# Kernel optimization log

Hardware: AMD Instinct MI355X
Metric: run time of the kernel (lower is better)

The kernel has to match this reference:

```python
import jax, jax.numpy as jnp
import numpy as np

N = 50000
E = 800000
NODE_F = 5
MAP_F = 32
EDGE_F = 4
HID = 64
RNN = 20
RNN_E = 8
LAT = 32
OUT = 4


def setup_inputs() -> dict:
    key = jax.random.key(0)
    ks = iter(jax.random.split(key, 40))
    def rn(shape, scale=0.1):
        return jax.random.normal(next(ks), shape, dtype=jnp.float32) * scale
    inp = {
        "x": rn((N, NODE_F), 1.0),
        "u": rn((N, MAP_F), 1.0),
        "edge_index": jax.random.randint(next(ks), (2, E), 0, N, dtype=jnp.int32),
        "edge_attr": rn((E, EDGE_F), 1.0),
        "h_node_h": rn((N, RNN), 1.0),
        "h_node_c": rn((N, RNN), 1.0),
        "h_edge_h": rn((N, RNN_E), 1.0),
        "h_edge_c": rn((N, RNN_E), 1.0),
        # node-history LSTM (input = node_features + map_encoding_size = 37)
        "W_ih_n": rn((4 * RNN, NODE_F + MAP_F)), "W_hh_n": rn((4 * RNN, RNN)),
        "b_ih_n": jnp.zeros((4 * RNN,), jnp.float32), "b_hh_n": jnp.zeros((4 * RNN,), jnp.float32),
        # edge-history LSTM (input = latent_edge_features)
        "W_ih_e": rn((4 * RNN_E, LAT)), "W_hh_e": rn((4 * RNN_E, RNN_E)),
        "b_ih_e": jnp.zeros((4 * RNN_E,), jnp.float32), "b_hh_e": jnp.zeros((4 * RNN_E,), jnp.float32),
        # message edge MLP: in = 2*37 + 4 = 78 -> 64 -> 32
        "We1": rn((2 * (NODE_F + MAP_F) + EDGE_F, HID)), "be1": jnp.zeros((HID,), jnp.float32),
        "We2": rn((HID, LAT)), "be2": jnp.zeros((LAT,), jnp.float32),
        # GN_out edge MLP: in = 2*(rnn_size + rnn_edge_size) + 4 = 60 -> 64 -> 32
        "Wo1": rn((2 * (RNN + RNN_E) + EDGE_F, HID)), "bo1": jnp.zeros((HID,), jnp.float32),
        "Wo2": rn((HID, LAT)), "bo2": jnp.zeros((LAT,), jnp.float32),
        # GN_out node MLP: in = (rnn_size + rnn_edge_size) + latent = 60 -> 64 -> 4
        "Wn1": rn((RNN + RNN_E + LAT, HID)), "bn1": jnp.zeros((HID,), jnp.float32),
        "Wn2": rn((HID, OUT)), "bn2": jnp.zeros((OUT,), jnp.float32),
    }
    return inp


def _lstm_step(xin, h, c, Wih, Whh, bih, bhh):
    # torch gate order: i, f, g, o
    g = xin @ Wih.T + h @ Whh.T + bih + bhh
    i, f, gg, o = jnp.split(g, 4, axis=-1)
    c_new = jax.nn.sigmoid(f) * c + jax.nn.sigmoid(i) * jnp.tanh(gg)
    h_new = jax.nn.sigmoid(o) * jnp.tanh(c_new)
    return h_new, c_new


def _segment_mean(vals, idx, n):
    s = jax.ops.segment_sum(vals, idx, num_segments=n)
    cnt = jax.ops.segment_sum(jnp.ones((vals.shape[0], 1), vals.dtype), idx, num_segments=n)
    return s / jnp.maximum(cnt, 1.0)


def _edge_mlp(src, dst, edge_attr, W1, b1, W2, b2):
    h = jnp.concatenate([src, dst, edge_attr], axis=-1)
    return jax.nn.relu(h @ W1 + b1) @ W2 + b2


def reference(x, u, edge_index, edge_attr, h_node_h, h_node_c, h_edge_h, h_edge_c,
              W_ih_n, W_hh_n, b_ih_n, b_hh_n, W_ih_e, W_hh_e, b_ih_e, b_hh_e,
              We1, be1, We2, be2, Wo1, bo1, Wo2, bo2, Wn1, bn1, Wn2, bn2):
    n = x.shape[0]
    xu = jnp.concatenate([x, u], axis=-1)  # [N, 37]
    # node history RNN step
    node_hist, node_c = _lstm_step(xu, h_node_h, h_node_c, W_ih_n, W_hh_n, b_ih_n, b_hh_n)
    # message GN: gather -> edge MLP
    row, col = edge_index[0], edge_index[1]
    messages = _edge_mlp(xu[row], xu[col], edge_attr, We1, be1, We2, be2)  # [E, 32]
    # edge history RNN: aggregate messages per receiving node, then LSTM step
    agg_msg = _segment_mean(messages, col, n)  # [N, 32]
    edge_hist, edge_c = _lstm_step(agg_msg, h_edge_h, h_edge_c, W_ih_e, W_hh_e, b_ih_e, b_hh_e)
    # output GN block
    full = jnp.concatenate([node_hist, edge_hist], axis=-1)  # [N, 28]
    e2 = _edge_mlp(full[row], full[col], edge_attr, Wo1, bo1, Wo2, bo2)  # [E, 32]
    agg2 = _segment_mean(e2, col, n)  # [N, 32]
    node_in = jnp.concatenate([full, agg2], axis=-1)  # [N, 60]
    out = jax.nn.relu(node_in @ Wn1 + bn1) @ Wn2 + bn2  # [N, 4]
    return (out, node_hist, node_c, edge_hist, edge_c)
```

## Files before the change

kernel.cpp:

```cpp
#include <hip/hip_runtime.h>
#include <math.h>

#define NN 50000
#define EE 800000
#define SBLK ((NN + 255) / 256)

typedef short bf16x8 __attribute__((ext_vector_type(8)));
typedef float f32x4 __attribute__((ext_vector_type(4)));
typedef unsigned short ushort_t;
#define MFMA16(a, b, c) __builtin_amdgcn_mfma_f32_16x16x32_bf16(a, b, c, 0, 0, 0)

__device__ __forceinline__ float sigmoidf_(float x) { return 1.0f / (1.0f + __expf(-x)); }

__device__ __forceinline__ unsigned short f2bf(float f) {
    unsigned u = __builtin_bit_cast(unsigned, f);
    u += 0x7FFFu + ((u >> 16) & 1u);
    return (unsigned short)(u >> 16);
}
__device__ __forceinline__ float bf2f(unsigned short v) {
    unsigned u = (unsigned)v << 16;
    return __builtin_bit_cast(float, u);
}
__device__ __forceinline__ unsigned pk2(float a, float b) {
    return ((unsigned)f2bf(b) << 16) | (unsigned)f2bf(a);
}

#define W1ST_A 104
#define W1ST_B 72
#define C1ST_  72
#define PW1A (64 * W1ST_A)
#define PW2A (32 * C1ST_)
#define PW1B (64 * W1ST_B)
#define PW2B (32 * C1ST_)

__global__ __launch_bounds__(256) void pack_w_k(
    const float* __restrict__ We1, const float* __restrict__ We2,
    const float* __restrict__ Wo1, const float* __restrict__ Wo2,
    ushort_t* __restrict__ pw)
{
    ushort_t* pw1a = pw;
    ushort_t* pw2a = pw1a + PW1A;
    ushort_t* pw1b = pw2a + PW2A;
    ushort_t* pw2b = pw1b + PW1B;
    int tid = threadIdx.x;

    for (int i = tid; i < PW1A; i += 256) {
        int n = i / W1ST_A, nk = i - n * W1ST_A;
        int kp = 0; bool z = false;
        if (nk < 37) kp = nk;
        else if (nk < 40) z = true;
        else if (nk < 77) kp = nk - 3;
        else if (nk < 80) z = true;
        else if (nk < 84) kp = nk - 6;
        else z = true;
        pw1a[i] = z ? (ushort_t)0 : f2bf(We1[kp * 64 + n]);
    }
    for (int i = tid; i < PW2A; i += 256) {
        int n = i / C1ST_, k = i - n * C1ST_;
        pw2a[i] = (k < 64) ? f2bf(We2[k * 32 + n]) : (ushort_t)0;
    }
    for (int i = tid; i < PW1B; i += 256) {
        int n = i / W1ST_B, nk = i - n * W1ST_B;
        int kp = 0; bool z = false;
        if (nk < 28) kp = nk;
        else if (nk < 32) z = true;
        else if (nk < 64) kp = nk - 4;
        else z = true;
        pw1b[i] = z ? (ushort_t)0 : f2bf(Wo1[kp * 64 + n]);
    }
    for (int i = tid; i < PW2B; i += 256) {
        int n = i / C1ST_, k = i - n * C1ST_;
        pw2b[i] = (k < 64) ? f2bf(Wo2[k * 32 + n]) : (ushort_t)0;
    }
}

__global__ __launch_bounds__(256) void node_lstm_k(
    const float* __restrict__ x, const float* __restrict__ u,
    const float* __restrict__ h0, const float* __restrict__ c0,
    const float* __restrict__ Wih, const float* __restrict__ Whh,
    const float* __restrict__ bih, const float* __restrict__ bhh,
    ushort_t* __restrict__ xu16, float* __restrict__ h_out, float* __restrict__ c_out)
{
    __shared__ float sWih[80 * 37];
    __shared__ float sWhh[80 * 20];
    __shared__ float sb[80];
    for (int i = threadIdx.x; i < 80 * 37; i += 256) sWih[i] = Wih[i];
    for (int i = threadIdx.x; i < 80 * 20; i += 256) sWhh[i] = Whh[i];
    if (threadIdx.x < 80) sb[threadIdx.x] = bih[threadIdx.x] + bhh[threadIdx.x];
    __syncthreads();
    int n = blockIdx.x * 256 + threadIdx.x;
    if (n >= NN) return;

    float xu[40];
#pragma unroll
    for (int k = 0; k < 5; k++) xu[k] = x[n * 5 + k];
#pragma unroll
    for (int k = 0; k < 32; k++) xu[5 + k] = u[n * 32 + k];
    xu[37] = 0.f; xu[38] = 0.f; xu[39] = 0.f;

    {
        unsigned w[20];
#pragma unroll
        for (int k = 0; k < 20; k++) w[k] = pk2(xu[2 * k], xu[2 * k + 1]);
        uint4* dst = (uint4*)(xu16 + (size_t)n * 40);
#pragma unroll
        for (int q = 0; q < 5; q++)
            dst[q] = make_uint4(w[q * 4], w[q * 4 + 1], w[q * 4 + 2], w[q * 4 + 3]);
    }

    float h[20];
#pragma unroll
    for (int k = 0; k < 20; k++) h[k] = h0[n * 20 + k];

#pragma unroll 1
    for (int r = 0; r < 20; r++) {
        float gi = sb[r], gf = sb[20 + r], gg = sb[40 + r], go = sb[60 + r];
#pragma unroll
        for (int k = 0; k < 37; k++) {
            float v = xu[k];
            gi = fmaf(v, sWih[r * 37 + k], gi);
            gf = fmaf(v, sWih[(20 + r) * 37 + k], gf);
            gg = fmaf(v, sWih[(40 + r) * 37 + k], gg);
            go = fmaf(v, sWih[(60 + r) * 37 + k], go);
        }
#pragma unroll
        for (int k = 0; k < 20; k++) {
            float v = h[k];
            gi = fmaf(v, sWhh[r * 20 + k], gi);
            gf = fmaf(v, sWhh[(20 + r) * 20 + k], gf);
            gg = fmaf(v, sWhh[(40 + r) * 20 + k], gg);
            go = fmaf(v, sWhh[(60 + r) * 20 + k], go);
        }
        float cr = c0[n * 20 + r];
        float cn = sigmoidf_(gf) * cr + sigmoidf_(gi) * tanhf(gg);
        float hn = sigmoidf_(go) * tanhf(cn);
        h_out[n * 20 + r] = hn;
        c_out[n * 20 + r] = cn;
    }
}

__global__ __launch_bounds__(256) void csr_count_k(const int* __restrict__ col,
                                                   int* __restrict__ count)
{
    int e = blockIdx.x * 256 + threadIdx.x;
    if (e < EE) atomicAdd(&count[col[e]], 1);
}

__global__ __launch_bounds__(256) void scan1_k(const int* __restrict__ count,
                                               int* __restrict__ bsum)
{
    __shared__ int red[256];
    int t = threadIdx.x;
    int i = blockIdx.x * 256 + t;
    red[t] = (i < NN) ? count[i] : 0;
    __syncthreads();
#pragma unroll
    for (int d = 128; d > 0; d >>= 1) {
        if (t < d) red[t] += red[t + d];
        __syncthreads();
    }
    if (t == 0) bsum[blockIdx.x] = red[0];
}

__global__ __launch_bounds__(256) void scan2_k(const int* __restrict__ bsum,
                                               int* __restrict__ bpre)
{
    __shared__ int s[256];
    int t = threadIdx.x;
    int v = (t < SBLK) ? bsum[t] : 0;
    s[t] = v;
    __syncthreads();
#pragma unroll
    for (int d = 1; d < 256; d <<= 1) {
        int w = (t >= d) ? s[t - d] : 0;
        __syncthreads();
        s[t] += w;
        __syncthreads();
    }
    if (t < SBLK) bpre[t] = s[t] - v;
}

__global__ __launch_bounds__(256) void scan3_k(const int* __restrict__ count,
                                               const int* __restrict__ bpre,
                                               int* __restrict__ offset,
                                               float* __restrict__ cntf)
{
    __shared__ int s[256];
    int t = threadIdx.x;
    int i = blockIdx.x * 256 + t;
    int v = (i < NN) ? count[i] : 0;
    s[t] = v;
    __syncthreads();
#pragma unroll
    for (int d = 1; d < 256; d <<= 1) {
        int w = (t >= d) ? s[t - d] : 0;
        __syncthreads();
        s[t] += w;
        __syncthreads();
    }
    if (i < NN) {
        offset[i] = bpre[blockIdx.x] + s[t] - v;
        cntf[i] = (float)v;
    }
}

__global__ __launch_bounds__(256) void csr_fill4_k(const int* __restrict__ row,
                                                   const int* __restrict__ col,
                                                   const float* __restrict__ eattr,
                                                   const int* __restrict__ offset,
                                                   int* __restrict__ cursor,
                                                   uint4* __restrict__ edat)
{
    int e = blockIdx.x * 256 + threadIdx.x;
    if (e >= EE) return;
    int c = col[e];
    int pos = atomicAdd(&cursor[c], 1);
    int slot = offset[c] + pos;
    float4 ev = *(const float4*)&eattr[(size_t)e * 4];
    edat[slot] = make_uint4((unsigned)row[e], (unsigned)c, pk2(ev.x, ev.y), pk2(ev.z, ev.w));
}

template <int F, int STRIDE, int INK>
__global__ __launch_bounds__(256, 4) void edge_mlp_fused_k(
    const ushort_t* __restrict__ feat,
    const uint4* __restrict__ edat,
    const int* __restrict__ offset, const int* __restrict__ count,
    const ushort_t* __restrict__ pw,
    const float* __restrict__ b1, const float* __restrict__ b2,
    float* __restrict__ agg)
{
    constexpr int S1 = INK / 32;
    constexpr int W1ST = INK + 8;
    constexpr int C1ST = C1ST_;
    constexpr int ABYTES = (64 * W1ST + 32 * C1ST + 4 * 32 * C1ST) * 2;
    constexpr int BBYTES = 32 * 257 * 4;
    constexpr int UBYTES = (ABYTES > BBYTES) ? ABYTES : BBYTES;
    constexpr int NU4 = (64 * W1ST + 32 * C1ST) / 8;

    __shared__ __align__(16) char ldsu[UBYTES];
    __shared__ int colLds[256];
    __shared__ unsigned char segStartA[256];
    __shared__ short segEndA[256];
    __shared__ int segCnt;

    ushort_t* sW1 = (ushort_t*)ldsu;
    ushort_t* sW2 = sW1 + 64 * W1ST;
    ushort_t* sC1 = sW2 + 32 * C1ST;
    float*    msgT = (float*)ldsu;

    const int tid = threadIdx.x;
    const int B0 = blockIdx.x * 256;
    if (tid == 0) segCnt = 0;
    colLds[tid] = (int)edat[B0 + tid].y;

    {
        const uint4* src = (const uint4*)pw;
        uint4* dst = (uint4*)ldsu;
        for (int i = tid; i < NU4; i += 256) dst[i] = src[i];
    }
    __syncthreads();

    {
        bool isStart = (tid == 0) || (colLds[tid] != colLds[tid - 1]);
        if (isStart) {
            int node = colLds[tid];
            int off = offset[node], cn = count[node];
            int e = off + cn - B0; if (e > 256) e = 256;
            bool fullseg = (off >= B0) && (off + cn <= B0 + 256);
            int j = atomicAdd(&segCnt, 1);
            segStartA[j] = (unsigned char)tid;
            segEndA[j] = (short)(fullseg ? -e : e);
        }
    }

    const int wave = tid >> 6, lane = tid & 63;
    const int lr = lane & 15, jb = lane >> 4;
    const size_t slotBase = (size_t)B0 + (size_t)wave * 64;
    const float4* b1v = (const float4*)b1;
    ushort_t* myC1 = sC1 + wave * 32 * C1ST;
    const float bb2_0 = b2[lr], bb2_1 = b2[16 + lr];

    f32x4 acc2a[2][2][2];

#pragma unroll
    for (int half = 0; half < 2; half++) {
        bf16x8 xf[2][S1];
#pragma unroll
        for (int ne2 = 0; ne2 < 2; ne2++) {
            size_t slot = slotBase + (size_t)(half * 2 + ne2) * 16 + lr;
            uint4 ed = edat[slot];
            const ushort_t* xr = feat + (size_t)ed.x * STRIDE;
            const ushort_t* xc = feat + (size_t)ed.y * STRIDE;
            xf[ne2][0] = *(const bf16x8*)(xr + jb * 8);
            if (F == 37) {
                const ushort_t* p1 = (jb == 0) ? (xr + 32) : (xc + (jb - 1) * 8);
                xf[ne2][1] = *(const bf16x8*)p1;
                bf16x8 v;
                if (jb < 2) {
                    v = *(const bf16x8*)((jb == 0) ? (xc + 24) : (xc + 32));
                } else if (jb == 2) {
                    uint4 t = make_uint4(ed.z, ed.w, 0u, 0u);
                    v = __builtin_bit_cast(bf16x8, t);
                } else {
                    uint4 t = make_uint4(0u, 0u, 0u, 0u);
                    v = __builtin_bit_cast(bf16x8, t);
                }
                xf[ne2][2] = v;
            } else {
                if (jb < 3) {
                    xf[ne2][1] = *(const bf16x8*)(xc + jb * 8);
                } else {
                    uint2 lo = *(const uint2*)(xc + 24);
                    uint4 t = make_uint4(lo.x, lo.y, ed.z, ed.w);
                    xf[ne2][1] = __builtin_bit_cast(bf16x8, t);
                }
            }
        }

        f32x4 acc1[4][2];
#pragma unroll
        for (int mh = 0; mh < 4; mh++) {
            float4 bv = b1v[mh * 4 + jb];
            f32x4 bi = {bv.x, bv.y, bv.z, bv.w};
            acc1[mh][0] = bi; acc1[mh][1] = bi;
        }
#pragma unroll
        for (int s = 0; s < S1; s++) {
#pragma unroll
            for (int mh = 0; mh < 4; mh++) {
                bf16x8 wf = *(const bf16x8*)&sW1[(mh * 16 + lr) * W1ST + s * 32 + jb * 8];
                acc1[mh][0] = MFMA16(wf, xf[0][s], acc1[mh][0]);
                acc1[mh][1] = MFMA16(wf, xf[1][s], acc1[mh][1]);
            }
        }

#pragma unroll
        for (int mh = 0; mh < 4; mh++) {
#pragma unroll
            for (int ne2 = 0; ne2 < 2; ne2++) {
                f32x4 a = acc1[mh][ne2];
                unsigned w0 = pk2(fmaxf(a[0], 0.f), fmaxf(a[1], 0.f));
                unsigned w1 = pk2(fmaxf(a[2], 0.f), fmaxf(a[3], 0.f));
                *(uint2*)&myC1[(ne2 * 16 + lr) * C1ST + mh * 16 + jb * 4] = make_uint2(w0, w1);
            }
        }

#pragma unroll
        for (int m = 0; m < 2; m++) {
            acc2a[half][m][0] = f32x4{bb2_0, bb2_0, bb2_0, bb2_0};
            acc2a[half][m][1] = f32x4{bb2_1, bb2_1, bb2_1, bb2_1};
        }
#pragma unroll
        for (int s2 = 0; s2 < 2; s2++) {
            bf16x8 w2f0 = *(const bf16x8*)&sW2[lr * C1ST + s2 * 32 + jb * 8];
            bf16x8 w2f1 = *(const bf16x8*)&sW2[(16 + lr) * C1ST + s2 * 32 + jb * 8];
#pragma unroll
            for (int m = 0; m < 2; m++) {
                bf16x8 a2 = *(const bf16x8*)&myC1[(m * 16 + lr) * C1ST + s2 * 32 + jb * 8];
                acc2a[half][m][0] = MFMA16(a2, w2f0, acc2a[half][m][0]);
                acc2a[half][m][1] = MFMA16(a2, w2f1, acc2a[half][m][1]);
            }
        }
    }

    __syncthreads();
#pragma unroll
    for (int half = 0; half < 2; half++) {
#pragma unroll
        for (int m = 0; m < 2; m++) {
            int row = wave * 64 + (half * 2 + m) * 16 + jb * 4;
#pragma unroll
            for (int n = 0; n < 2; n++) {
                f32x4 a = acc2a[half][m][n];
                float* dst = &msgT[(size_t)(n * 16 + lr) * 257 + row];
                dst[0] = a[0]; dst[1] = a[1]; dst[2] = a[2]; dst[3] = a[3];
            }
        }
    }
    __syncthreads();

    {
        int f = lane & 31;
        int h = lane >> 5;
        const float* mrow = msgT + (size_t)f * 257;
        int nseg = segCnt;
        for (int j = wave; j < nseg; j += 4) {
            int s = segStartA[j];
            int ev = segEndA[j];
            bool fullseg = ev < 0;
            int e = fullseg ? -ev : ev;
            int node = colLds[s];
            float sum = 0.f;
            for (int i = s + h; i < e; i += 2) sum += mrow[i];
            sum += __shfl_xor(sum, 32);
            if (lane < 32) {
                float* dst = &agg[(size_t)node * 32 + f];
                if (fullseg) *dst = sum;
                else atomicAdd(dst, sum);
            }
        }
    }
}

__global__ __launch_bounds__(256) void edge_lstm_k(
    const float* __restrict__ agg, const float* __restrict__ cnt,
    const float* __restrict__ h0, const float* __restrict__ c0,
    const float* __restrict__ Wih, const float* __restrict__ Whh,
    const float* __restrict__ bih, const float* __restrict__ bhh,
    const float* __restrict__ node_h,
    float* __restrict__ h_out, float* __restrict__ c_out, ushort_t* __restrict__ full16)
{
    __shared__ float sWih[32 * 32];
    __shared__ float sWhh[32 * 8];
    __shared__ float sb[32];
    for (int i = threadIdx.x; i < 32 * 32; i += 256) sWih[i] = Wih[i];
    for (int i = threadIdx.x; i < 32 * 8; i += 256) sWhh[i] = Whh[i];
    if (threadIdx.x < 32) sb[threadIdx.x] = bih[threadIdx.x] + bhh[threadIdx.x];
    __syncthreads();
    int n = blockIdx.x * 256 + threadIdx.x;
    if (n >= NN) return;

    float inv = 1.0f / fmaxf(cnt[n], 1.0f);
    float msg[32];
#pragma unroll
    for (int k = 0; k < 32; k++) msg[k] = agg[(size_t)n * 32 + k] * inv;
    float h[8];
#pragma unroll
    for (int k = 0; k < 8; k++) h[k] = h0[n * 8 + k];

    float fl[32];
#pragma unroll
    for (int k = 0; k < 20; k++) fl[k] = node_h[n * 20 + k];
    fl[28] = 0.f; fl[29] = 0.f; fl[30] = 0.f; fl[31] = 0.f;

#pragma unroll
    for (int r = 0; r < 8; r++) {
        float gi = sb[r], gf = sb[8 + r], gg = sb[16 + r], go = sb[24 + r];
#pragma unroll
        for (int k = 0; k < 32; k++) {
            float v = msg[k];
            gi = fmaf(v, sWih[r * 32 + k], gi);
            gf = fmaf(v, sWih[(8 + r) * 32 + k], gf);
            gg = fmaf(v, sWih[(16 + r) * 32 + k], gg);
            go = fmaf(v, sWih[(24 + r) * 32 + k], go);
        }
#pragma unroll
        for (int k = 0; k < 8; k++) {
            float v = h[k];
            gi = fmaf(v, sWhh[r * 8 + k], gi);
            gf = fmaf(v, sWhh[(8 + r) * 8 + k], gf);
            gg = fmaf(v, sWhh[(16 + r) * 8 + k], gg);
            go = fmaf(v, sWhh[(24 + r) * 8 + k], go);
        }
        float cr = c0[n * 8 + r];
        float cn = sigmoidf_(gf) * cr + sigmoidf_(gi) * tanhf(gg);
        float hn = sigmoidf_(go) * tanhf(cn);
        h_out[n * 8 + r] = hn;
        c_out[n * 8 + r] = cn;
        fl[20 + r] = hn;
    }
    unsigned w[16];
#pragma unroll
    for (int k = 0; k < 16; k++) w[k] = pk2(fl[2 * k], fl[2 * k + 1]);
    uint4* dst = (uint4*)(full16 + (size_t)n * 32);
#pragma unroll
    for (int q = 0; q < 4; q++)
        dst[q] = make_uint4(w[q * 4], w[q * 4 + 1], w[q * 4 + 2], w[q * 4 + 3]);
}

__global__ __launch_bounds__(256) void node_out_k(
    const ushort_t* __restrict__ full16, const float* __restrict__ agg2, const float* __restrict__ cnt,
    const float* __restrict__ W1, const float* __restrict__ b1,
    const float* __restrict__ W2, const float* __restrict__ b2,
    float* __restrict__ out)
{
    __shared__ __align__(16) float sW1[60 * 64];
    __shared__ __align__(16) float sW2[64 * 4];
    __shared__ float sb1[64];
    __shared__ float sb2[4];
    for (int i = threadIdx.x; i < 60 * 64; i += 256) sW1[i] = W1[i];
    for (int i = threadIdx.x; i < 64 * 4; i += 256) sW2[i] = W2[i];
    if (threadIdx.x < 64) sb1[threadIdx.x] = b1[threadIdx.x];
    if (threadIdx.x < 4) sb2[threadIdx.x] = b2[threadIdx.x];
    __syncthreads();
    int n = blockIdx.x * 256 + threadIdx.x;
    if (n >= NN) return;

    float in[60];
    const ushort_t* fr = full16 + (size_t)n * 32;
#pragma unroll
    for (int k = 0; k < 28; k++) in[k] = bf2f(fr[k]);
    float inv = 1.0f / fmaxf(cnt[n], 1.0f);
#pragma unroll
    for (int k = 0; k < 32; k++) in[28 + k] = agg2[(size_t)n * 32 + k] * inv;

    float o[4] = {sb2[0], sb2[1], sb2[2], sb2[3]};
#pragma unroll 1
    for (int j = 0; j < 64; j += 4) {
        float s[4] = {sb1[j], sb1[j + 1], sb1[j + 2], sb1[j + 3]};
#pragma unroll
        for (int k = 0; k < 60; k++) {
            float4 w = *(const float4*)&sW1[k * 64 + j];
            s[0] = fmaf(in[k], w.x, s[0]);
            s[1] = fmaf(in[k], w.y, s[1]);
            s[2] = fmaf(in[k], w.z, s[2]);
            s[3] = fmaf(in[k], w.w, s[3]);
        }
#pragma unroll
        for (int jj = 0; jj < 4; jj++) {
            float sv = fmaxf(s[jj], 0.0f);
            float4 w = *(const float4*)&sW2[(j + jj) * 4];
            o[0] = fmaf(sv, w.x, o[0]);
            o[1] = fmaf(sv, w.y, o[1]);
            o[2] = fmaf(sv, w.z, o[2]);
            o[3] = fmaf(sv, w.w, o[3]);
        }
    }
#pragma unroll
    for (int m = 0; m < 4; m++) out[n * 4 + m] = o[m];
}

template <int F, int STRIDE, bool DO_CNT>
__global__ __launch_bounds__(256) void edge_mlp_atomic_k(
    const ushort_t* __restrict__ feat,
    const int* __restrict__ row, const int* __restrict__ col,
    const float* __restrict__ eattr,
    const float* __restrict__ W1, const float* __restrict__ b1,
    const float* __restrict__ W2, const float* __restrict__ b2,
    float* __restrict__ agg, float* __restrict__ cnt)
{
    constexpr int IN = 2 * F + 4;
    __shared__ __align__(16) float sW1[IN * 64];
    __shared__ __align__(16) float sW2[64 * 32];
    __shared__ float sb1[64];
    __shared__ float sb2[32];
    for (int i = threadIdx.x; i < IN * 64; i += 256) sW1[i] = W1[i];
    for (int i = threadIdx.x; i < 64 * 32; i += 256) sW2[i] = W2[i];
    if (threadIdx.x < 64) sb1[threadIdx.x] = b1[threadIdx.x];
    if (threadIdx.x < 32) sb2[threadIdx.x] = b2[threadIdx.x];
    __syncthreads();
    int e = blockIdx.x * 256 + threadIdx.x;
    if (e >= EE) return;

    int r = row[e], c = col[e];
    float h[IN];
#pragma unroll
    for (int k = 0; k < F; k++) h[k] = bf2f(feat[(size_t)r * STRIDE + k]);
#pragma unroll
    for (int k = 0; k < F; k++) h[F + k] = bf2f(feat[(size_t)c * STRIDE + k]);
    float4 ev = *(const float4*)&eattr[(size_t)e * 4];
    h[2 * F] = ev.x; h[2 * F + 1] = ev.y; h[2 * F + 2] = ev.z; h[2 * F + 3] = ev.w;

    float out[32];
#pragma unroll
    for (int m = 0; m < 32; m++) out[m] = sb2[m];
#pragma unroll 1
    for (int j = 0; j < 64; j += 4) {
        float s[4] = {sb1[j], sb1[j + 1], sb1[j + 2], sb1[j + 3]};
#pragma unroll
        for (int k = 0; k < IN; k++) {
            float4 w = *(const float4*)&sW1[k * 64 + j];
            s[0] = fmaf(h[k], w.x, s[0]);
            s[1] = fmaf(h[k], w.y, s[1]);
            s[2] = fmaf(h[k], w.z, s[2]);
            s[3] = fmaf(h[k], w.w, s[3]);
        }
        s[0] = fmaxf(s[0], 0.f); s[1] = fmaxf(s[1], 0.f);
        s[2] = fmaxf(s[2], 0.f); s[3] = fmaxf(s[3], 0.f);
#pragma unroll
        for (int jj = 0; jj < 4; jj++) {
#pragma unroll
            for (int m = 0; m < 32; m += 4) {
                float4 w = *(const float4*)&sW2[(j + jj) * 32 + m];
                out[m]     = fmaf(s[jj], w.x, out[m]);
                out[m + 1] = fmaf(s[jj], w.y, out[m + 1]);
                out[m + 2] = fmaf(s[jj], w.z, out[m + 2]);
                out[m + 3] = fmaf(s[jj], w.w, out[m + 3]);
            }
        }
    }
    float* dst = &agg[(size_t)c * 32];
#pragma unroll
    for (int m = 0; m < 32; m++) atomicAdd(&dst[m], out[m]);
    if (DO_CNT) atomicAdd(&cnt[c], 1.0f);
}

extern "C" void kernel_launch(void* const* d_in, const int* in_sizes, int n_in,
                              void* d_out, int out_size, void* d_ws, size_t ws_size,
                              hipStream_t stream) {
    (void)in_sizes; (void)n_in; (void)out_size;
    const float* x      = (const float*)d_in[0];
    const float* u      = (const float*)d_in[1];
    const int*   ei     = (const int*)d_in[2];
    const float* eattr  = (const float*)d_in[3];
    const float* hn_h   = (const float*)d_in[4];
    const float* hn_c   = (const float*)d_in[5];
    const float* he_h   = (const float*)d_in[6];
    const float* he_c   = (const float*)d_in[7];
    const float* Wih_n  = (const float*)d_in[8];
    const float* Whh_n  = (const float*)d_in[9];
    const float* bih_n  = (const float*)d_in[10];
    const float* bhh_n  = (const float*)d_in[11];
    const float* Wih_e  = (const float*)d_in[12];
    const float* Whh_e  = (const float*)d_in[13];
    const float* bih_e  = (const float*)d_in[14];
    const float* bhh_e  = (const float*)d_in[15];
    const float* We1    = (const float*)d_in[16];
    const float* be1    = (const float*)d_in[17];
    const float* We2    = (const float*)d_in[18];
    const float* be2    = (const float*)d_in[19];
    const float* Wo1    = (const float*)d_in[20];
    const float* bo1    = (const float*)d_in[21];
    const float* Wo2    = (const float*)d_in[22];
    const float* bo2    = (const float*)d_in[23];
    const float* Wn1    = (const float*)d_in[24];
    const float* bn1    = (const float*)d_in[25];
    const float* Wn2    = (const float*)d_in[26];
    const float* bn2    = (const float*)d_in[27];

    const int* row = ei;
    const int* col = ei + EE;

    float* out = (float*)d_out;
    float* out_y   = out;
    float* node_h  = out + (size_t)NN * 4;
    float* node_c  = out + (size_t)NN * 24;
    float* edge_h  = out + (size_t)NN * 44;
    float* edge_c  = out + (size_t)NN * 52;

    int nb_n = (NN + 255) / 256;
    int nb_e = (EE + 255) / 256;

    ushort_t* xu16   = (ushort_t*)d_ws;
    ushort_t* full16 = xu16 + (size_t)NN * 40;
    float* agg  = (float*)(full16 + (size_t)NN * 32);
    float* cntf = agg + (size_t)NN * 32;
    float* agg2 = cntf + NN;
    int* count  = (int*)(agg2 + (size_t)NN * 32);
    int* cursor = count + NN;
    int* offset = cursor + NN;
    int* bsum   = offset + NN;
    int* bpre   = bsum + SBLK;
    size_t pw_off = ((size_t)((char*)(bpre + SBLK) - (char*)d_ws) + 15) & ~(size_t)15;
    ushort_t* pw = (ushort_t*)((char*)d_ws + pw_off);
    size_t edat_off = ((pw_off + (size_t)(PW1A + PW2A + PW1B + PW2B) * 2) + 15) & ~(size_t)15;
    uint4* edat = (uint4*)((char*)d_ws + edat_off);
    size_t needed = edat_off + (size_t)EE * 16;

    if (ws_size >= needed) {
        hipMemsetAsync(agg, 0, (size_t)NN * (32 + 1 + 32 + 1 + 1) * sizeof(float), stream);

        pack_w_k<<<1, 256, 0, stream>>>(We1, We2, Wo1, Wo2, pw);
        node_lstm_k<<<nb_n, 256, 0, stream>>>(x, u, hn_h, hn_c, Wih_n, Whh_n, bih_n, bhh_n,
                                              xu16, node_h, node_c);
        csr_count_k<<<nb_e, 256, 0, stream>>>(col, count);
        scan1_k<<<SBLK, 256, 0, stream>>>(count, bsum);
        scan2_k<<<1, 256, 0, stream>>>(bsum, bpre);
        scan3_k<<<SBLK, 256, 0, stream>>>(count, bpre, offset, cntf);
        csr_fill4_k<<<nb_e, 256, 0, stream>>>(row, col, eattr, offset, cursor, edat);

        edge_mlp_fused_k<37, 40, 96><<<EE / 256, 256, 0, stream>>>(
            xu16, edat, offset, count, pw, be1, be2, agg);
        edge_lstm_k<<<nb_n, 256, 0, stream>>>(agg, cntf, he_h, he_c, Wih_e, Whh_e, bih_e, bhh_e,
                                              node_h, edge_h, edge_c, full16);
        edge_mlp_fused_k<28, 32, 64><<<EE / 256, 256, 0, stream>>>(
            full16, edat, offset, count, pw + PW1A + PW2A, bo1, bo2, agg2);
        node_out_k<<<nb_n, 256, 0, stream>>>(full16, agg2, cntf, Wn1, bn1, Wn2, bn2, out_y);
    } else {
        hipMemsetAsync(agg, 0, (size_t)NN * (32 + 1 + 32) * sizeof(float), stream);
        node_lstm_k<<<nb_n, 256, 0, stream>>>(x, u, hn_h, hn_c, Wih_n, Whh_n, bih_n, bhh_n,
                                              xu16, node_h, node_c);
        edge_mlp_atomic_k<37, 40, true><<<nb_e, 256, 0, stream>>>(xu16, row, col, eattr,
                                                                  We1, be1, We2, be2, agg, cntf);
        edge_lstm_k<<<nb_n, 256, 0, stream>>>(agg, cntf, he_h, he_c, Wih_e, Whh_e, bih_e, bhh_e,
                                              node_h, edge_h, edge_c, full16);
        edge_mlp_atomic_k<28, 32, false><<<nb_e, 256, 0, stream>>>(full16, row, col, eattr,
                                                                   Wo1, bo1, Wo2, bo2, agg2, nullptr);
        node_out_k<<<nb_n, 256, 0, stream>>>(full16, agg2, cntf, Wn1, bn1, Wn2, bn2, out_y);
    }
}
```

Baseline: 261.5 us.

## Replace packed per-edge CSR records with edge-id permutation and sorted col array

Instead of scattering a 16-byte record (row, col, bf16 attrs) per edge into CSR order, the fill kernel now writes only a 4-byte edge id. Sorted col indices are written by the scan kernel, and attributes are converted to bf16 in original order during counting. The edge MLP kernels then read row and attributes indirectly through the edge id. This cuts scattered write traffic during CSR build, but adds dependent random gathers (row[e], ea16[e]) in both edge MLP passes. The scan kernel also gains a serial per-node loop to fill the sorted col array.

```diff
diff --git a/kernel.cpp b/kernel.cpp
--- a/kernel.cpp
+++ b/kernel.cpp
@@ -139,11 +139,16 @@
     }
 }
 
-__global__ __launch_bounds__(256) void csr_count_k(const int* __restrict__ col,
-                                                   int* __restrict__ count)
+__global__ __launch_bounds__(256) void csr_count_cvt_k(const int* __restrict__ col,
+                                                       const float* __restrict__ eattr,
+                                                       int* __restrict__ count,
+                                                       ushort_t* __restrict__ ea16)
 {
     int e = blockIdx.x * 256 + threadIdx.x;
-    if (e < EE) atomicAdd(&count[col[e]], 1);
+    if (e >= EE) return;
+    atomicAdd(&count[col[e]], 1);
+    float4 ev = *(const float4*)&eattr[(size_t)e * 4];
+    *(uint2*)&ea16[(size_t)e * 4] = make_uint2(pk2(ev.x, ev.y), pk2(ev.z, ev.w));
 }
 
 __global__ __launch_bounds__(256) void scan1_k(const int* __restrict__ count,
@@ -183,7 +188,8 @@
 __global__ __launch_bounds__(256) void scan3_k(const int* __restrict__ count,
                                                const int* __restrict__ bpre,
                                                int* __restrict__ offset,
-                                               float* __restrict__ cntf)
+                                               float* __restrict__ cntf,
+                                               int* __restrict__ colp)
 {
     __shared__ int s[256];
     int t = threadIdx.x;
@@ -199,31 +205,30 @@
         __syncthreads();
     }
     if (i < NN) {
-        offset[i] = bpre[blockIdx.x] + s[t] - v;
+        int off = bpre[blockIdx.x] + s[t] - v;
+        offset[i] = off;
         cntf[i] = (float)v;
-    }
-}
-
-__global__ __launch_bounds__(256) void csr_fill4_k(const int* __restrict__ row,
-                                                   const int* __restrict__ col,
-                                                   const float* __restrict__ eattr,
-                                                   const int* __restrict__ offset,
-                                                   int* __restrict__ cursor,
-                                                   uint4* __restrict__ edat)
+        for (int j = 0; j < v; j++) colp[off + j] = i;
+    }
+}
+
+__global__ __launch_bounds__(256) void csr_fill_eid_k(const int* __restrict__ col,
+                                                      const int* __restrict__ offset,
+                                                      int* __restrict__ cursor,
+                                                      int* __restrict__ eid)
 {
     int e = blockIdx.x * 256 + threadIdx.x;
     if (e >= EE) return;
     int c = col[e];
     int pos = atomicAdd(&cursor[c], 1);
-    int slot = offset[c] + pos;
-    float4 ev = *(const float4*)&eattr[(size_t)e * 4];
-    edat[slot] = make_uint4((unsigned)row[e], (unsigned)c, pk2(ev.x, ev.y), pk2(ev.z, ev.w));
+    eid[offset[c] + pos] = e;
 }
 
 template <int F, int STRIDE, int INK>
 __global__ __launch_bounds__(256, 4) void edge_mlp_fused_k(
     const ushort_t* __restrict__ feat,
-    const uint4* __restrict__ edat,
+    const int* __restrict__ eid, const int* __restrict__ colp,
+    const ushort_t* __restrict__ ea16, const int* __restrict__ rowArr,
     const int* __restrict__ offset, const int* __restrict__ count,
     const ushort_t* __restrict__ pw,
     const float* __restrict__ b1, const float* __restrict__ b2,
@@ -251,7 +256,7 @@
     const int tid = threadIdx.x;
     const int B0 = blockIdx.x * 256;
     if (tid == 0) segCnt = 0;
-    colLds[tid] = (int)edat[B0 + tid].y;
+    colLds[tid] = colp[B0 + tid];
 
     {
         const uint4* src = (const uint4*)pw;
@@ -288,9 +293,9 @@
 #pragma unroll
         for (int ne2 = 0; ne2 < 2; ne2++) {
             size_t slot = slotBase + (size_t)(half * 2 + ne2) * 16 + lr;
-            uint4 ed = edat[slot];
-            const ushort_t* xr = feat + (size_t)ed.x * STRIDE;
-            const ushort_t* xc = feat + (size_t)ed.y * STRIDE;
+            int e = eid[slot];
+            const ushort_t* xr = feat + (size_t)rowArr[e] * STRIDE;
+            const ushort_t* xc = feat + (size_t)colLds[slot - B0] * STRIDE;
             xf[ne2][0] = *(const bf16x8*)(xr + jb * 8);
             if (F == 37) {
                 const ushort_t* p1 = (jb == 0) ? (xr + 32) : (xc + (jb - 1) * 8);
@@ -299,7 +304,8 @@
                 if (jb < 2) {
                     v = *(const bf16x8*)((jb == 0) ? (xc + 24) : (xc + 32));
                 } else if (jb == 2) {
-                    uint4 t = make_uint4(ed.z, ed.w, 0u, 0u);
+                    uint2 ea = *(const uint2*)&ea16[(size_t)e * 4];
+                    uint4 t = make_uint4(ea.x, ea.y, 0u, 0u);
                     v = __builtin_bit_cast(bf16x8, t);
                 } else {
                     uint4 t = make_uint4(0u, 0u, 0u, 0u);
@@ -311,7 +317,8 @@
                     xf[ne2][1] = *(const bf16x8*)(xc + jb * 8);
                 } else {
                     uint2 lo = *(const uint2*)(xc + 24);
-                    uint4 t = make_uint4(lo.x, lo.y, ed.z, ed.w);
+                    uint2 ea = *(const uint2*)&ea16[(size_t)e * 4];
+                    uint4 t = make_uint4(lo.x, lo.y, ea.x, ea.y);
                     xf[ne2][1] = __builtin_bit_cast(bf16x8, t);
                 }
             }
@@ -643,9 +650,12 @@
     int* bpre   = bsum + SBLK;
     size_t pw_off = ((size_t)((char*)(bpre + SBLK) - (char*)d_ws) + 15) & ~(size_t)15;
     ushort_t* pw = (ushort_t*)((char*)d_ws + pw_off);
-    size_t edat_off = ((pw_off + (size_t)(PW1A + PW2A + PW1B + PW2B) * 2) + 15) & ~(size_t)15;
-    uint4* edat = (uint4*)((char*)d_ws + edat_off);
-    size_t needed = edat_off + (size_t)EE * 16;
+    size_t eid_off = ((pw_off + (size_t)(PW1A + PW2A + PW1B + PW2B) * 2) + 15) & ~(size_t)15;
+    int* eid  = (int*)((char*)d_ws + eid_off);
+    int* colp = eid + EE;
+    size_t ea_off = ((size_t)((char*)(colp + EE) - (char*)d_ws) + 15) & ~(size_t)15;
+    ushort_t* ea16 = (ushort_t*)((char*)d_ws + ea_off);
+    size_t needed = ea_off + (size_t)EE * 4 * sizeof(ushort_t);
 
     if (ws_size >= needed) {
         hipMemsetAsync(agg, 0, (size_t)NN * (32 + 1 + 32 + 1 + 1) * sizeof(float), stream);
@@ -653,18 +663,18 @@
         pack_w_k<<<1, 256, 0, stream>>>(We1, We2, Wo1, Wo2, pw);
         node_lstm_k<<<nb_n, 256, 0, stream>>>(x, u, hn_h, hn_c, Wih_n, Whh_n, bih_n, bhh_n,
                                               xu16, node_h, node_c);
-        csr_count_k<<<nb_e, 256, 0, stream>>>(col, count);
+        csr_count_cvt_k<<<nb_e, 256, 0, stream>>>(col, eattr, count, ea16);
         scan1_k<<<SBLK, 256, 0, stream>>>(count, bsum);
         scan2_k<<<1, 256, 0, stream>>>(bsum, bpre);
-        scan3_k<<<SBLK, 256, 0, stream>>>(count, bpre, offset, cntf);
-        csr_fill4_k<<<nb_e, 256, 0, stream>>>(row, col, eattr, offset, cursor, edat);
+        scan3_k<<<SBLK, 256, 0, stream>>>(count, bpre, offset, cntf, colp);
+        csr_fill_eid_k<<<nb_e, 256, 0, stream>>>(col, offset, cursor, eid);
 
         edge_mlp_fused_k<37, 40, 96><<<EE / 256, 256, 0, stream>>>(
-            xu16, edat, offset, count, pw, be1, be2, agg);
+            xu16, eid, colp, ea16, row, offset, count, pw, be1, be2, agg);
         edge_lstm_k<<<nb_n, 256, 0, stream>>>(agg, cntf, he_h, he_c, Wih_e, Whh_e, bih_e, bhh_e,
                                               node_h, edge_h, edge_c, full16);
         edge_mlp_fused_k<28, 32, 64><<<EE / 256, 256, 0, stream>>>(
-            full16, edat, offset, count, pw + PW1A + PW2A, bo1, bo2, agg2);
+            full16, eid, colp, ea16, row, offset, count, pw + PW1A + PW2A, bo1, bo2, agg2);
         node_out_k<<<nb_n, 256, 0, stream>>>(full16, agg2, cntf, Wn1, bn1, Wn2, bn2, out_y);
     } else {
         hipMemsetAsync(agg, 0, (size_t)NN * (32 + 1 + 32) * sizeof(float), stream);
```

New measurement: 302.8 us. 15.8% more time.

## Shrink edge-MLP LDS and registers to raise occupancy with bf16 message staging

Applied to the files above, without the earlier changes.

The fused edge-MLP kernel now processes one 16-edge group at a time instead of two, which halves the per-wave layer-1 scratch and the live accumulator registers. Messages are staged in LDS as bf16 instead of fp32, shrinking the transposed buffer so the union LDS footprint is smaller. The launch bound is raised from 4 to 5 blocks per SM to use the freed resources for occupancy. In exchange, MFMA weight-fragment reuse across two edge groups is lost, and rounding messages to bf16 before the segment sum adds precision error.

```diff
diff --git a/kernel.cpp b/kernel.cpp
--- a/kernel.cpp
+++ b/kernel.cpp
@@ -221,7 +221,7 @@
 }
 
 template <int F, int STRIDE, int INK>
-__global__ __launch_bounds__(256, 4) void edge_mlp_fused_k(
+__global__ __launch_bounds__(256, 5) void edge_mlp_fused_k(
     const ushort_t* __restrict__ feat,
     const uint4* __restrict__ edat,
     const int* __restrict__ offset, const int* __restrict__ count,
@@ -232,8 +232,9 @@
     constexpr int S1 = INK / 32;
     constexpr int W1ST = INK + 8;
     constexpr int C1ST = C1ST_;
-    constexpr int ABYTES = (64 * W1ST + 32 * C1ST + 4 * 32 * C1ST) * 2;
-    constexpr int BBYTES = 32 * 257 * 4;
+    constexpr int MST = 260;
+    constexpr int ABYTES = (64 * W1ST + 32 * C1ST + 4 * 16 * C1ST) * 2;
+    constexpr int BBYTES = 32 * MST * 2;
     constexpr int UBYTES = (ABYTES > BBYTES) ? ABYTES : BBYTES;
     constexpr int NU4 = (64 * W1ST + 32 * C1ST) / 8;
 
@@ -246,7 +247,7 @@
     ushort_t* sW1 = (ushort_t*)ldsu;
     ushort_t* sW2 = sW1 + 64 * W1ST;
     ushort_t* sC1 = sW2 + 32 * C1ST;
-    float*    msgT = (float*)ldsu;
+    ushort_t* msgT16 = (ushort_t*)ldsu;
 
     const int tid = threadIdx.x;
     const int B0 = blockIdx.x * 256;
@@ -277,24 +278,23 @@
     const int lr = lane & 15, jb = lane >> 4;
     const size_t slotBase = (size_t)B0 + (size_t)wave * 64;
     const float4* b1v = (const float4*)b1;
-    ushort_t* myC1 = sC1 + wave * 32 * C1ST;
+    ushort_t* myC1 = sC1 + wave * 16 * C1ST;
     const float bb2_0 = b2[lr], bb2_1 = b2[16 + lr];
 
-    f32x4 acc2a[2][2][2];
-
-#pragma unroll
-    for (int half = 0; half < 2; half++) {
-        bf16x8 xf[2][S1];
-#pragma unroll
-        for (int ne2 = 0; ne2 < 2; ne2++) {
-            size_t slot = slotBase + (size_t)(half * 2 + ne2) * 16 + lr;
+    f32x4 acc2a[4][2];
+
+#pragma unroll
+    for (int q = 0; q < 4; q++) {
+        bf16x8 xf[S1];
+        {
+            size_t slot = slotBase + (size_t)q * 16 + lr;
             uint4 ed = edat[slot];
             const ushort_t* xr = feat + (size_t)ed.x * STRIDE;
             const ushort_t* xc = feat + (size_t)ed.y * STRIDE;
-            xf[ne2][0] = *(const bf16x8*)(xr + jb * 8);
+            xf[0] = *(const bf16x8*)(xr + jb * 8);
             if (F == 37) {
                 const ushort_t* p1 = (jb == 0) ? (xr + 32) : (xc + (jb - 1) * 8);
-                xf[ne2][1] = *(const bf16x8*)p1;
+                xf[1] = *(const bf16x8*)p1;
                 bf16x8 v;
                 if (jb < 2) {
                     v = *(const bf16x8*)((jb == 0) ? (xc + 24) : (xc + 32));
@@ -305,76 +305,62 @@
                     uint4 t = make_uint4(0u, 0u, 0u, 0u);
                     v = __builtin_bit_cast(bf16x8, t);
                 }
-                xf[ne2][2] = v;
+                xf[2] = v;
             } else {
                 if (jb < 3) {
-                    xf[ne2][1] = *(const bf16x8*)(xc + jb * 8);
+                    xf[1] = *(const bf16x8*)(xc + jb * 8);
                 } else {
                     uint2 lo = *(const uint2*)(xc + 24);
                     uint4 t = make_uint4(lo.x, lo.y, ed.z, ed.w);
-                    xf[ne2][1] = __builtin_bit_cast(bf16x8, t);
+                    xf[1] = __builtin_bit_cast(bf16x8, t);
                 }
             }
         }
 
-        f32x4 acc1[4][2];
+        f32x4 acc1[4];
 #pragma unroll
         for (int mh = 0; mh < 4; mh++) {
             float4 bv = b1v[mh * 4 + jb];
-            f32x4 bi = {bv.x, bv.y, bv.z, bv.w};
-            acc1[mh][0] = bi; acc1[mh][1] = bi;
+            acc1[mh] = f32x4{bv.x, bv.y, bv.z, bv.w};
         }
 #pragma unroll
         for (int s = 0; s < S1; s++) {
 #pragma unroll
             for (int mh = 0; mh < 4; mh++) {
                 bf16x8 wf = *(const bf16x8*)&sW1[(mh * 16 + lr) * W1ST + s * 32 + jb * 8];
-                acc1[mh][0] = MFMA16(wf, xf[0][s], acc1[mh][0]);
-                acc1[mh][1] = MFMA16(wf, xf[1][s], acc1[mh][1]);
+                acc1[mh] = MFMA16(wf, xf[s], acc1[mh]);
             }
         }
 
 #pragma unroll
         for (int mh = 0; mh < 4; mh++) {
-#pragma unroll
-            for (int ne2 = 0; ne2 < 2; ne2++) {
-                f32x4 a = acc1[mh][ne2];
-                unsigned w0 = pk2(fmaxf(a[0], 0.f), fmaxf(a[1], 0.f));
-                unsigned w1 = pk2(fmaxf(a[2], 0.f), fmaxf(a[3], 0.f));
-                *(uint2*)&myC1[(ne2 * 16 + lr) * C1ST + mh * 16 + jb * 4] = make_uint2(w0, w1);
-            }
-        }
-
-#pragma unroll
-        for (int m = 0; m < 2; m++) {
-            acc2a[half][m][0] = f32x4{bb2_0, bb2_0, bb2_0, bb2_0};
-            acc2a[half][m][1] = f32x4{bb2_1, bb2_1, bb2_1, bb2_1};
-        }
+            f32x4 a = acc1[mh];
+            unsigned w0 = pk2(fmaxf(a[0], 0.f), fmaxf(a[1], 0.f));
+            unsigned w1 = pk2(fmaxf(a[2], 0.f), fmaxf(a[3], 0.f));
+            *(uint2*)&myC1[(jb * 4 + 0) * 0 + lr * C1ST + mh * 16 + jb * 4] = make_uint2(w0, w1);
+        }
+
+        acc2a[q][0] = f32x4{bb2_0, bb2_0, bb2_0, bb2_0};
+        acc2a[q][1] = f32x4{bb2_1, bb2_1, bb2_1, bb2_1};
 #pragma unroll
         for (int s2 = 0; s2 < 2; s2++) {
             bf16x8 w2f0 = *(const bf16x8*)&sW2[lr * C1ST + s2 * 32 + jb * 8];
             bf16x8 w2f1 = *(const bf16x8*)&sW2[(16 + lr) * C1ST + s2 * 32 + jb * 8];
-#pragma unroll
-            for (int m = 0; m < 2; m++) {
-                bf16x8 a2 = *(const bf16x8*)&myC1[(m * 16 + lr) * C1ST + s2 * 32 + jb * 8];
-                acc2a[half][m][0] = MFMA16(a2, w2f0, acc2a[half][m][0]);
-                acc2a[half][m][1] = MFMA16(a2, w2f1, acc2a[half][m][1]);
-            }
-        }
-    }
-
-    __syncthreads();
-#pragma unroll
-    for (int half = 0; half < 2; half++) {
-#pragma unroll
-        for (int m = 0; m < 2; m++) {
-            int row = wave * 64 + (half * 2 + m) * 16 + jb * 4;
-#pragma unroll
-            for (int n = 0; n < 2; n++) {
-                f32x4 a = acc2a[half][m][n];
-                float* dst = &msgT[(size_t)(n * 16 + lr) * 257 + row];
-                dst[0] = a[0]; dst[1] = a[1]; dst[2] = a[2]; dst[3] = a[3];
-            }
+            bf16x8 a2 = *(const bf16x8*)&myC1[lr * C1ST + s2 * 32 + jb * 8];
+            acc2a[q][0] = MFMA16(a2, w2f0, acc2a[q][0]);
+            acc2a[q][1] = MFMA16(a2, w2f1, acc2a[q][1]);
+        }
+    }
+
+    __syncthreads();
+#pragma unroll
+    for (int q = 0; q < 4; q++) {
+        int row = wave * 64 + q * 16 + jb * 4;
+#pragma unroll
+        for (int n = 0; n < 2; n++) {
+            f32x4 a = acc2a[q][n];
+            ushort_t* dst = &msgT16[(size_t)(n * 16 + lr) * MST + row];
+            *(uint2*)dst = make_uint2(pk2(a[0], a[1]), pk2(a[2], a[3]));
         }
     }
     __syncthreads();
@@ -382,7 +368,7 @@
     {
         int f = lane & 31;
         int h = lane >> 5;
-        const float* mrow = msgT + (size_t)f * 257;
+        const ushort_t* mrow = msgT16 + (size_t)f * MST;
         int nseg = segCnt;
         for (int j = wave; j < nseg; j += 4) {
             int s = segStartA[j];
@@ -391,7 +377,7 @@
             int e = fullseg ? -ev : ev;
             int node = colLds[s];
             float sum = 0.f;
-            for (int i = s + h; i < e; i += 2) sum += mrow[i];
+            for (int i = s + h; i < e; i += 2) sum += bf2f(mrow[i]);
             sum += __shfl_xor(sum, 32);
             if (lane < 32) {
                 float* dst = &agg[(size_t)node * 32 + f];
```

New measurement: 261.6 us. No clear change (+0.0%).
